# Performance work log

Measured on AMD Instinct MI355X. Metric: run time of the kernel, lower is better.

## Reference

```python
import jax, jax.numpy as jnp
import numpy as np
from jax import lax

B, S, D, H = 4, 1024, 1024, 16
DK = D // H


def setup_inputs() -> dict:
    key = jax.random.key(0)
    ks = jax.random.split(key, 8)
    s = 0.02
    return {
        "text_embeddings": jax.random.normal(ks[0], (B, S, D), jnp.float32),
        "text_mask": jnp.ones((B, S), jnp.int32),
        "W_G": jax.random.normal(ks[1], (D, D), jnp.float32) * s,
        "b_G": jnp.zeros((D,), jnp.float32),
        "Wq": jax.random.normal(ks[2], (D, D), jnp.float32) * s,
        "bq": jnp.zeros((D,), jnp.float32),
        "Wk": jax.random.normal(ks[3], (D, D), jnp.float32) * s,
        "bk": jnp.zeros((D,), jnp.float32),
        "conv_w": jax.random.normal(ks[4], (D, H, 3), jnp.float32) * s,
        "conv_b": jnp.zeros((D,), jnp.float32),
    }


def _rope_tables(seq_len, dk):
    # interleaved sinusoidal tables, each value repeated twice along feature dim
    pos = jnp.arange(seq_len, dtype=jnp.float32)[:, None]            # [S,1]
    inv = jnp.power(10000.0, -2.0 * jnp.arange(dk // 2, dtype=jnp.float32) / dk)
    ang = pos * inv                                                   # [S,DK/2]
    cos_pos = jnp.repeat(jnp.cos(ang), 2, axis=-1)[None, None]        # [1,1,S,DK]
    sin_pos = jnp.repeat(jnp.sin(ang), 2, axis=-1)[None, None]
    return cos_pos, sin_pos


def reference(text_embeddings, text_mask, W_G, b_G, Wq, bq, Wk, bk, conv_w, conv_b):
    b, s, d = text_embeddings.shape
    g = text_embeddings @ W_G + b_G                                   # [B,S,D]
    q = (g @ Wq + bq).reshape(b, s, H, DK).transpose(0, 2, 1, 3)      # [B,H,S,DK]
    k = (g @ Wk + bk).reshape(b, s, H, DK).transpose(0, 2, 1, 3)

    cos_pos, sin_pos = _rope_tables(s, DK)
    # NOTE: query rotation uses +q_odd (module does NOT negate for q), key uses -k_odd
    qw2 = jnp.stack([q[..., 1::2], q[..., ::2]], axis=-1).reshape(q.shape)
    qw = q * cos_pos + qw2 * sin_pos
    kw2 = jnp.stack([-k[..., 1::2], k[..., ::2]], axis=-1).reshape(k.shape)
    kw = k * cos_pos + kw2 * sin_pos

    scores = jnp.einsum("bhqd,bhkd->bhqk", qw, kw) / np.float32(np.sqrt(DK))
    mask = text_mask[:, None, None, :]                                # [B,1,1,S]
    scores = jnp.where(mask == 0, jnp.float32(-1e9), scores)
    p_attn = jax.nn.softmax(scores, axis=-1)                          # [B,H,S,S]

    row0 = p_attn[:, :, 0, :]                                         # [B,H,S]
    conv = lax.conv_general_dilated(
        row0, conv_w, window_strides=(1,), padding=[(1, 1)],
        dimension_numbers=("NCH", "OIH", "NCH"))                      # [B,D,S]
    return jax.nn.relu(conv + conv_b[None, :, None])
```

## Files before the change

### kernel.cpp

```cpp
#include <hip/hip_runtime.h>
#include <math.h>

#define B_  4
#define S_  1024
#define D_  1024
#define H_  16
#define DK_ 64
#define M_  (B_ * S_)

typedef __bf16 bf16x8 __attribute__((ext_vector_type(8)));
typedef float  f32x4  __attribute__((ext_vector_type(4)));

__device__ __forceinline__ unsigned short f2bf(float f) {
  unsigned u = __builtin_bit_cast(unsigned, f);
  u = (u + 0x7FFFu + ((u >> 16) & 1u)) >> 16;
  return (unsigned short)u;
}
__device__ __forceinline__ float bf2f(unsigned short h) {
  unsigned u = ((unsigned)h) << 16;
  return __builtin_bit_cast(float, u);
}

__device__ __forceinline__ void gl_lds16(const void* g, void* lds) {
  __builtin_amdgcn_global_load_lds(
      (const __attribute__((address_space(1))) unsigned int*)(unsigned long long)g,
      (__attribute__((address_space(3))) unsigned int*)(unsigned int)(unsigned long long)lds,
      16, 0, 0);
}

__global__ __launch_bounds__(256) void prep_kernel(
    const float* __restrict__ X, const float* __restrict__ W_G,
    const float* __restrict__ Wk, unsigned short* __restrict__ Xbf,
    unsigned short* __restrict__ WGT, unsigned short* __restrict__ WkT,
    float* __restrict__ tab) {
  __shared__ float tle[32][33];
  const int blk = blockIdx.x;
  const int tid = threadIdx.x;

  if (blk < 2048) {
    const int i = (blk * 256 + tid) * 2;
    const float4 v0 = ((const float4*)X)[i];
    const float4 v1 = ((const float4*)X)[i + 1];
    ushort4 h0, h1;
    h0.x = f2bf(v0.x); h0.y = f2bf(v0.y); h0.z = f2bf(v0.z); h0.w = f2bf(v0.w);
    h1.x = f2bf(v1.x); h1.y = f2bf(v1.y); h1.z = f2bf(v1.z); h1.w = f2bf(v1.w);
    ((ushort4*)Xbf)[i] = h0;
    ((ushort4*)Xbf)[i + 1] = h1;
  } else if (blk < 4096) {
    const bool isG = blk < 3072;
    const float* W = isG ? W_G : Wk;
    unsigned short* WT = isG ? WGT : WkT;
    const int t = isG ? blk - 2048 : blk - 3072;
    const int k0 = (t & 31) * 32;
    const int n0 = (t >> 5) * 32;
    const int tx = tid & 31;
    const int ty = tid >> 5;
#pragma unroll
    for (int r = 0; r < 32; r += 8)
      tle[ty + r][tx] = W[(size_t)(k0 + ty + r) * 1024 + n0 + tx];
    __syncthreads();
#pragma unroll
    for (int r = 0; r < 32; r += 8)
      WT[(size_t)(n0 + ty + r) * 1024 + k0 + tx] = f2bf(tle[tx][ty + r]);
  } else {
    const int idx = (blk - 4096) * 256 + tid;
    const int s = idx >> 5, j = idx & 31;
    const float inv = (float)exp(-(double)j * (9.210340371976182736 / 32.0));
    float sn, c;
    sincosf((float)s * inv, &sn, &c);
    tab[(size_t)s * 64 + 2 * j] = c;
    tab[(size_t)s * 64 + 2 * j + 1] = sn;
  }
}

#define GM 64
#define GN 128

__global__ __launch_bounds__(256) void gemm_bf16(
    const unsigned short* __restrict__ A, const unsigned short* __restrict__ BT,
    const float* __restrict__ bias, unsigned short* __restrict__ C,
    const float* __restrict__ Wq, float* __restrict__ part, int nGemmBlocks) {
  __shared__ __align__(16) unsigned short As[2][GM * 32];
  __shared__ __align__(16) unsigned short Bs[2][GN * 32];
  __shared__ float gs[4][32];

  const int flat = blockIdx.x;
  const int tid  = threadIdx.x;

  if (flat >= nGemmBlocks) {
    const int qb = flat - nGemmBlocks;
    const int slab = qb >> 2;
    const int n = (qb & 3) * 256 + tid;
    if (tid < 128) {
      const int b = tid >> 5, kk = tid & 31;
      gs[b][kk] = bf2f(A[(size_t)b * S_ * D_ + slab * 32 + kk]);
    }
    __syncthreads();
    float a0 = 0.f, a1 = 0.f, a2 = 0.f, a3 = 0.f;
#pragma unroll
    for (int kk = 0; kk < 32; ++kk) {
      const float w = Wq[(size_t)(slab * 32 + kk) * D_ + n];
      a0 = fmaf(gs[0][kk], w, a0);
      a1 = fmaf(gs[1][kk], w, a1);
      a2 = fmaf(gs[2][kk], w, a2);
      a3 = fmaf(gs[3][kk], w, a3);
    }
    part[(size_t)(slab * 4 + 0) * D_ + n] = a0;
    part[(size_t)(slab * 4 + 1) * D_ + n] = a1;
    part[(size_t)(slab * 4 + 2) * D_ + n] = a2;
    part[(size_t)(slab * 4 + 3) * D_ + n] = a3;
    return;
  }

  const int bx = flat & 7;
  const int by = flat >> 3;
  const int wv   = tid >> 6;
  const int lane = tid & 63;
  const int m0 = by * GM;
  const int n0 = bx * GN;

  const int colOff = (lane & 3) * 8;
  const size_t aOff  = (size_t)(m0 + 16 * wv + (lane >> 2)) * 1024 + colOff;
  const size_t bOff0 = (size_t)(n0 + 32 * wv + (lane >> 2)) * 1024 + colOff;
  const size_t bOff1 = bOff0 + (size_t)16 * 1024;

  const int l15  = lane & 15;
  const int quad = lane >> 4;

  f32x4 acc[4][2];
#pragma unroll
  for (int i = 0; i < 4; ++i)
#pragma unroll
    for (int j = 0; j < 2; ++j) acc[i][j] = (f32x4){0.f, 0.f, 0.f, 0.f};

#pragma unroll 1
  for (int k0 = 0; k0 < 1024; k0 += 64) {
    __syncthreads();
#pragma unroll
    for (int ks = 0; ks < 2; ++ks) {
      gl_lds16(A  + aOff  + k0 + ks * 32, &As[ks][wv * 512]);
      gl_lds16(BT + bOff0 + k0 + ks * 32, &Bs[ks][wv * 1024]);
      gl_lds16(BT + bOff1 + k0 + ks * 32, &Bs[ks][wv * 1024 + 512]);
    }
    __syncthreads();

#pragma unroll
    for (int ks = 0; ks < 2; ++ks) {
      bf16x8 af[4], bfr[2];
#pragma unroll
      for (int mi = 0; mi < 4; ++mi)
        af[mi] = *(const bf16x8*)(&As[ks][(mi * 16 + l15) * 32 + quad * 8]);
#pragma unroll
      for (int ni = 0; ni < 2; ++ni)
        bfr[ni] =
            *(const bf16x8*)(&Bs[ks][(wv * 32 + ni * 16 + l15) * 32 + quad * 8]);
#pragma unroll
      for (int mi = 0; mi < 4; ++mi)
#pragma unroll
        for (int ni = 0; ni < 2; ++ni)
          acc[mi][ni] = __builtin_amdgcn_mfma_f32_16x16x32_bf16(
              af[mi], bfr[ni], acc[mi][ni], 0, 0, 0);
    }
  }

#pragma unroll
  for (int ni = 0; ni < 2; ++ni) {
    const int n = n0 + wv * 32 + ni * 16 + l15;
    const float bv = bias[n];
#pragma unroll
    for (int mi = 0; mi < 4; ++mi) {
#pragma unroll
      for (int r = 0; r < 4; ++r) {
        const int m = m0 + mi * 16 + quad * 4 + r;
        C[(size_t)m * 1024 + n] = f2bf(acc[mi][ni][r] + bv);
      }
    }
  }
}

__global__ __launch_bounds__(256) void attn_scores_kernel(
    const unsigned short* __restrict__ Kbf, const float* __restrict__ part,
    const float* __restrict__ bq, const float* __restrict__ tab,
    const int* __restrict__ mask, float* __restrict__ scores,
    float* __restrict__ mS) {
  const int bi = blockIdx.x;
  const int b = bi >> 9;
  const int h = (bi >> 5) & 15;
  const int chunk = bi & 31;
  const int tid = threadIdx.x;
  const int bh = b * H_ + h;
  const int sl = tid >> 3;
  const int j  = tid & 7;
  const int s  = chunk * 32 + sl;

  __shared__ float q0s[DK_];
  __shared__ float wredm[4];
  __shared__ float wreds[4];

  if (tid < 64) {
    const int n = h * DK_ + tid;
    float v = bq[n];
#pragma unroll
    for (int sl2 = 0; sl2 < 32; ++sl2)
      v += part[(size_t)(sl2 * 4 + b) * D_ + n];
    q0s[tid] = v;
  }
  __syncthreads();

  const ushort4* kp =
      (const ushort4*)(Kbf + ((size_t)(b * S_ + s)) * D_ + h * DK_ + j * 8);
  const ushort4 k0 = kp[0], k1 = kp[1];
  const float4* tb = (const float4*)(tab + (size_t)s * 64 + j * 8);
  const float4 t0 = tb[0], t1 = tb[1];

  float dot = 0.f;
  {
    const float ka = bf2f(k0.x), kb = bf2f(k0.y);
    dot += q0s[j * 8 + 0] * (ka * t0.x - kb * t0.y) +
           q0s[j * 8 + 1] * (kb * t0.x + ka * t0.y);
  }
  {
    const float ka = bf2f(k0.z), kb = bf2f(k0.w);
    dot += q0s[j * 8 + 2] * (ka * t0.z - kb * t0.w) +
           q0s[j * 8 + 3] * (kb * t0.z + ka * t0.w);
  }
  {
    const float ka = bf2f(k1.x), kb = bf2f(k1.y);
    dot += q0s[j * 8 + 4] * (ka * t1.x - kb * t1.y) +
           q0s[j * 8 + 5] * (kb * t1.x + ka * t1.y);
  }
  {
    const float ka = bf2f(k1.z), kb = bf2f(k1.w);
    dot += q0s[j * 8 + 6] * (ka * t1.z - kb * t1.w) +
           q0s[j * 8 + 7] * (kb * t1.z + ka * t1.w);
  }
  dot += __shfl_xor(dot, 1);
  dot += __shfl_xor(dot, 2);
  dot += __shfl_xor(dot, 4);
  dot *= 0.125f;
  if (mask[b * S_ + s] == 0) dot = -1e9f;
  if (j == 0) scores[(size_t)bh * S_ + s] = dot;

  float mx = dot;
#pragma unroll
  for (int off = 8; off < 64; off <<= 1) mx = fmaxf(mx, __shfl_xor(mx, off));
  if ((tid & 63) == 0) wredm[tid >> 6] = mx;
  __syncthreads();
  mx = fmaxf(fmaxf(wredm[0], wredm[1]), fmaxf(wredm[2], wredm[3]));

  float e = (j == 0) ? expf(dot - mx) : 0.f;
#pragma unroll
  for (int off = 1; off < 64; off <<= 1) e += __shfl_xor(e, off);
  if ((tid & 63) == 0) wreds[tid >> 6] = e;
  __syncthreads();
  if (tid == 0) {
    mS[(size_t)(bh * 32 + chunk) * 2 + 0] = mx;
    mS[(size_t)(bh * 32 + chunk) * 2 + 1] =
        wreds[0] + wreds[1] + wreds[2] + wreds[3];
  }
}

__global__ __launch_bounds__(256) void conv_norm_relu_kernel(
    const float* __restrict__ scores, const float* __restrict__ mS,
    const float* __restrict__ cw, const float* __restrict__ cb,
    float* __restrict__ out) {
  const int b = blockIdx.y;
  const int s0 = blockIdx.x * 16;
  const int oz = blockIdx.z * 256;
  const int tid = threadIdx.x;

  __shared__ float msh[16], ish[16];
  __shared__ float sm[16][18];

  if (tid < 16) {
    const int bh = b * H_ + tid;
    float m = -3e38f;
#pragma unroll
    for (int c = 0; c < 32; ++c)
      m = fmaxf(m, mS[(size_t)(bh * 32 + c) * 2]);
    float S = 0.f;
#pragma unroll
    for (int c = 0; c < 32; ++c)
      S += mS[(size_t)(bh * 32 + c) * 2 + 1] *
           expf(mS[(size_t)(bh * 32 + c) * 2] - m);
    msh[tid] = m;
    ish[tid] = 1.f / S;
  }
  __syncthreads();

  for (int i = tid; i < 16 * 18; i += 256) {
    const int c = i / 18, ss = i % 18;
    const int gs = s0 - 1 + ss;
    float p = 0.f;
    if (gs >= 0 && gs < S_) {
      const int bh = b * H_ + c;
      p = expf(scores[(size_t)bh * S_ + gs] - msh[c]) * ish[c];
    }
    sm[c][ss] = p;
  }
  __syncthreads();

  const int og = tid >> 4;
  const int si = tid & 15;

  float r[16][3];
#pragma unroll
  for (int c = 0; c < 16; ++c) {
    r[c][0] = sm[c][si + 0];
    r[c][1] = sm[c][si + 1];
    r[c][2] = sm[c][si + 2];
  }

#pragma unroll 1
  for (int i = 0; i < 16; ++i) {
    const int o = oz + i * 16 + og;
    const float4* wo = (const float4*)(cw + (size_t)o * 48);
    float accv = cb[o];
#pragma unroll
    for (int q = 0; q < 12; ++q) {
      const float4 w4 = wo[q];
      const int f0 = q * 4;
      accv = fmaf(r[(f0 + 0) / 3][(f0 + 0) % 3], w4.x, accv);
      accv = fmaf(r[(f0 + 1) / 3][(f0 + 1) % 3], w4.y, accv);
      accv = fmaf(r[(f0 + 2) / 3][(f0 + 2) % 3], w4.z, accv);
      accv = fmaf(r[(f0 + 3) / 3][(f0 + 3) % 3], w4.w, accv);
    }
    out[((size_t)b * D_ + o) * S_ + s0 + si] = fmaxf(accv, 0.f);
  }
}

extern "C" void kernel_launch(void* const* d_in, const int* in_sizes, int n_in,
                              void* d_out, int out_size, void* d_ws,
                              size_t ws_size, hipStream_t stream) {
  const float* x    = (const float*)d_in[0];
  const int*   mask = (const int*)d_in[1];
  const float* W_G  = (const float*)d_in[2];
  const float* b_G  = (const float*)d_in[3];
  const float* Wq   = (const float*)d_in[4];
  const float* bq   = (const float*)d_in[5];
  const float* Wk   = (const float*)d_in[6];
  const float* bk   = (const float*)d_in[7];
  const float* cw   = (const float*)d_in[8];
  const float* cb   = (const float*)d_in[9];
  float* out = (float*)d_out;

  char* ws = (char*)d_ws;
  unsigned short* Xbf = (unsigned short*)(ws);
  unsigned short* G   = (unsigned short*)(ws + (8u << 20));
  unsigned short* Kbf = (unsigned short*)(ws + (16u << 20));
  unsigned short* WGT = (unsigned short*)(ws + (24u << 20));
  unsigned short* WkT = (unsigned short*)(ws + (26u << 20));
  float* part   = (float*)(ws + (28u << 20));
  float* ropeT  = (float*)(ws + (28u << 20) + (512u << 10));
  float* scores = (float*)(ws + (28u << 20) + (768u << 10));
  float* mS     = (float*)(ws + (28u << 20) + (1024u << 10));

  prep_kernel<<<4224, 256, 0, stream>>>(x, W_G, Wk, Xbf, WGT, WkT, ropeT);
  gemm_bf16<<<512, 256, 0, stream>>>(Xbf, WGT, b_G, G, nullptr, nullptr, 512);
  gemm_bf16<<<640, 256, 0, stream>>>(G, WkT, bk, Kbf, Wq, part, 512);
  attn_scores_kernel<<<2048, 256, 0, stream>>>(Kbf, part, bq, ropeT, mask,
                                               scores, mS);
  conv_norm_relu_kernel<<<dim3(S_ / 16, B_, 4), 256, 0, stream>>>(
      scores, mS, cw, cb, out);
}
```

Measured before the change: 163.2 us.

## Fuse all stages into one persistent kernel with grid barriers

Replaces the five separate launches (prep, two GEMMs, attention scores, conv) with a single persistent kernel of 512 blocks. Stages are separated by atomic-counter grid barriers, and each stage's work is grid-strided over the blocks. The softmax also drops its running-max subtraction and stores exp(score) and per-chunk sums directly. This removes launch gaps and the separate max reduction. The costs are barrier spin overhead, a q-projection tail that runs only on 128 blocks, and possible exp overflow for large scores.

```diff
diff --git a/kernel.cpp b/kernel.cpp
--- a/kernel.cpp
+++ b/kernel.cpp
@@ -7,6 +7,7 @@
 #define H_  16
 #define DK_ 64
 #define M_  (B_ * S_)
+#define NBLK 512
 
 typedef __bf16 bf16x8 __attribute__((ext_vector_type(8)));
 typedef float  f32x4  __attribute__((ext_vector_type(4)));
@@ -28,72 +29,167 @@
       16, 0, 0);
 }
 
-__global__ __launch_bounds__(256) void prep_kernel(
-    const float* __restrict__ X, const float* __restrict__ W_G,
-    const float* __restrict__ Wk, unsigned short* __restrict__ Xbf,
-    unsigned short* __restrict__ WGT, unsigned short* __restrict__ WkT,
-    float* __restrict__ tab) {
-  __shared__ float tle[32][33];
+__device__ __forceinline__ void grid_barrier(unsigned* ctr) {
+  __syncthreads();
+  if (threadIdx.x == 0) {
+    __threadfence();
+    atomicAdd(ctr, 1u);
+    while (__hip_atomic_load(ctr, __ATOMIC_ACQUIRE,
+                             __HIP_MEMORY_SCOPE_AGENT) < NBLK)
+      __builtin_amdgcn_s_sleep(1);
+    __threadfence();
+  }
+  __syncthreads();
+}
+
+__device__ __forceinline__ void gemm_tile(
+    const unsigned short* __restrict__ A, const unsigned short* __restrict__ BT,
+    const float* __restrict__ bias, unsigned short* __restrict__ C,
+    int flat, unsigned char* SMEM) {
+  unsigned short* As = (unsigned short*)SMEM;
+  unsigned short* Bs = (unsigned short*)(SMEM + 8192);
+
+  const int tid  = threadIdx.x;
+  const int bx = flat & 7;
+  const int by = flat >> 3;
+  const int wv   = tid >> 6;
+  const int lane = tid & 63;
+  const int m0 = by * 64;
+  const int n0 = bx * 128;
+
+  const int colOff = (lane & 3) * 8;
+  const size_t aOff  = (size_t)(m0 + 16 * wv + (lane >> 2)) * 1024 + colOff;
+  const size_t bOff0 = (size_t)(n0 + 32 * wv + (lane >> 2)) * 1024 + colOff;
+  const size_t bOff1 = bOff0 + (size_t)16 * 1024;
+
+  const int l15  = lane & 15;
+  const int quad = lane >> 4;
+
+  f32x4 acc[4][2];
+#pragma unroll
+  for (int i = 0; i < 4; ++i)
+#pragma unroll
+    for (int j = 0; j < 2; ++j) acc[i][j] = (f32x4){0.f, 0.f, 0.f, 0.f};
+
+#pragma unroll 1
+  for (int k0 = 0; k0 < 1024; k0 += 64) {
+    __syncthreads();
+#pragma unroll
+    for (int ks = 0; ks < 2; ++ks) {
+      gl_lds16(A  + aOff  + k0 + ks * 32, As + ks * 2048 + wv * 512);
+      gl_lds16(BT + bOff0 + k0 + ks * 32, Bs + ks * 4096 + wv * 1024);
+      gl_lds16(BT + bOff1 + k0 + ks * 32, Bs + ks * 4096 + wv * 1024 + 512);
+    }
+    __syncthreads();
+
+#pragma unroll
+    for (int ks = 0; ks < 2; ++ks) {
+      bf16x8 af[4], bfr[2];
+#pragma unroll
+      for (int mi = 0; mi < 4; ++mi)
+        af[mi] =
+            *(const bf16x8*)(As + ks * 2048 + (mi * 16 + l15) * 32 + quad * 8);
+#pragma unroll
+      for (int ni = 0; ni < 2; ++ni)
+        bfr[ni] = *(const bf16x8*)(Bs + ks * 4096 +
+                                   (wv * 32 + ni * 16 + l15) * 32 + quad * 8);
+#pragma unroll
+      for (int mi = 0; mi < 4; ++mi)
+#pragma unroll
+        for (int ni = 0; ni < 2; ++ni)
+          acc[mi][ni] = __builtin_amdgcn_mfma_f32_16x16x32_bf16(
+              af[mi], bfr[ni], acc[mi][ni], 0, 0, 0);
+    }
+  }
+
+#pragma unroll
+  for (int ni = 0; ni < 2; ++ni) {
+    const int n = n0 + wv * 32 + ni * 16 + l15;
+    const float bv = bias[n];
+#pragma unroll
+    for (int mi = 0; mi < 4; ++mi) {
+#pragma unroll
+      for (int r = 0; r < 4; ++r) {
+        const int m = m0 + mi * 16 + quad * 4 + r;
+        C[(size_t)m * 1024 + n] = f2bf(acc[mi][ni][r] + bv);
+      }
+    }
+  }
+}
+
+__global__ __launch_bounds__(256, 2) void mega_kernel(
+    const float* __restrict__ x, const int* __restrict__ mask,
+    const float* __restrict__ W_G, const float* __restrict__ b_G,
+    const float* __restrict__ Wq, const float* __restrict__ bq,
+    const float* __restrict__ Wk, const float* __restrict__ bk,
+    const float* __restrict__ cw, const float* __restrict__ cb,
+    unsigned short* __restrict__ Xbf, unsigned short* __restrict__ G,
+    unsigned short* __restrict__ Kbf, unsigned short* __restrict__ WGT,
+    unsigned short* __restrict__ WkT, float* __restrict__ part,
+    float* __restrict__ ropeT, float* __restrict__ scores,
+    float* __restrict__ mS, unsigned* __restrict__ bar,
+    float* __restrict__ out) {
+  __shared__ __align__(16) unsigned char SMEM[24576];
   const int blk = blockIdx.x;
   const int tid = threadIdx.x;
 
-  if (blk < 2048) {
-    const int i = (blk * 256 + tid) * 2;
-    const float4 v0 = ((const float4*)X)[i];
-    const float4 v1 = ((const float4*)X)[i + 1];
-    ushort4 h0, h1;
-    h0.x = f2bf(v0.x); h0.y = f2bf(v0.y); h0.z = f2bf(v0.z); h0.w = f2bf(v0.w);
-    h1.x = f2bf(v1.x); h1.y = f2bf(v1.y); h1.z = f2bf(v1.z); h1.w = f2bf(v1.w);
-    ((ushort4*)Xbf)[i] = h0;
-    ((ushort4*)Xbf)[i + 1] = h1;
-  } else if (blk < 4096) {
-    const bool isG = blk < 3072;
-    const float* W = isG ? W_G : Wk;
-    unsigned short* WT = isG ? WGT : WkT;
-    const int t = isG ? blk - 2048 : blk - 3072;
-    const int k0 = (t & 31) * 32;
-    const int n0 = (t >> 5) * 32;
-    const int tx = tid & 31;
-    const int ty = tid >> 5;
-#pragma unroll
-    for (int r = 0; r < 32; r += 8)
-      tle[ty + r][tx] = W[(size_t)(k0 + ty + r) * 1024 + n0 + tx];
+  {
+    float (*tle)[33] = (float(*)[33])SMEM;
+    for (int u = blk; u < 4224; u += NBLK) {
+      __syncthreads();
+      if (u < 2048) {
+        const int i = (u * 256 + tid) * 2;
+        const float4 v0 = ((const float4*)x)[i];
+        const float4 v1 = ((const float4*)x)[i + 1];
+        ushort4 h0, h1;
+        h0.x = f2bf(v0.x); h0.y = f2bf(v0.y);
+        h0.z = f2bf(v0.z); h0.w = f2bf(v0.w);
+        h1.x = f2bf(v1.x); h1.y = f2bf(v1.y);
+        h1.z = f2bf(v1.z); h1.w = f2bf(v1.w);
+        ((ushort4*)Xbf)[i] = h0;
+        ((ushort4*)Xbf)[i + 1] = h1;
+      } else if (u < 4096) {
+        const bool isG = u < 3072;
+        const float* W = isG ? W_G : Wk;
+        unsigned short* WT = isG ? WGT : WkT;
+        const int t = u - (isG ? 2048 : 3072);
+        const int k0 = (t & 31) * 32;
+        const int n0 = (t >> 5) * 32;
+        const int tx = tid & 31;
+        const int ty = tid >> 5;
+#pragma unroll
+        for (int r = 0; r < 32; r += 8)
+          tle[ty + r][tx] = W[(size_t)(k0 + ty + r) * 1024 + n0 + tx];
+        __syncthreads();
+#pragma unroll
+        for (int r = 0; r < 32; r += 8)
+          WT[(size_t)(n0 + ty + r) * 1024 + k0 + tx] = f2bf(tle[tx][ty + r]);
+      } else {
+        const int idx = (u - 4096) * 256 + tid;
+        const int s = idx >> 5, j = idx & 31;
+        const float inv =
+            (float)exp(-(double)j * (9.210340371976182736 / 32.0));
+        float sn, c;
+        sincosf((float)s * inv, &sn, &c);
+        ropeT[(size_t)s * 64 + 2 * j] = c;
+        ropeT[(size_t)s * 64 + 2 * j + 1] = sn;
+      }
+    }
+  }
+  grid_barrier(bar + 0);
+
+  gemm_tile(Xbf, WGT, b_G, G, blk, SMEM);
+  grid_barrier(bar + 1);
+
+  gemm_tile(G, WkT, bk, Kbf, blk, SMEM);
+  if (blk < 128) {
     __syncthreads();
-#pragma unroll
-    for (int r = 0; r < 32; r += 8)
-      WT[(size_t)(n0 + ty + r) * 1024 + k0 + tx] = f2bf(tle[tx][ty + r]);
-  } else {
-    const int idx = (blk - 4096) * 256 + tid;
-    const int s = idx >> 5, j = idx & 31;
-    const float inv = (float)exp(-(double)j * (9.210340371976182736 / 32.0));
-    float sn, c;
-    sincosf((float)s * inv, &sn, &c);
-    tab[(size_t)s * 64 + 2 * j] = c;
-    tab[(size_t)s * 64 + 2 * j + 1] = sn;
-  }
-}
-
-#define GM 64
-#define GN 128
-
-__global__ __launch_bounds__(256) void gemm_bf16(
-    const unsigned short* __restrict__ A, const unsigned short* __restrict__ BT,
-    const float* __restrict__ bias, unsigned short* __restrict__ C,
-    const float* __restrict__ Wq, float* __restrict__ part, int nGemmBlocks) {
-  __shared__ __align__(16) unsigned short As[2][GM * 32];
-  __shared__ __align__(16) unsigned short Bs[2][GN * 32];
-  __shared__ float gs[4][32];
-
-  const int flat = blockIdx.x;
-  const int tid  = threadIdx.x;
-
-  if (flat >= nGemmBlocks) {
-    const int qb = flat - nGemmBlocks;
-    const int slab = qb >> 2;
-    const int n = (qb & 3) * 256 + tid;
+    float (*gs)[32] = (float(*)[32])SMEM;
+    const int slab = blk >> 2;
+    const int n = (blk & 3) * 256 + tid;
     if (tid < 128) {
       const int b = tid >> 5, kk = tid & 31;
-      gs[b][kk] = bf2f(A[(size_t)b * S_ * D_ + slab * 32 + kk]);
+      gs[b][kk] = bf2f(G[(size_t)b * S_ * D_ + slab * 32 + kk]);
     }
     __syncthreads();
     float a0 = 0.f, a1 = 0.f, a2 = 0.f, a3 = 0.f;
@@ -109,223 +205,129 @@
     part[(size_t)(slab * 4 + 1) * D_ + n] = a1;
     part[(size_t)(slab * 4 + 2) * D_ + n] = a2;
     part[(size_t)(slab * 4 + 3) * D_ + n] = a3;
-    return;
-  }
-
-  const int bx = flat & 7;
-  const int by = flat >> 3;
-  const int wv   = tid >> 6;
-  const int lane = tid & 63;
-  const int m0 = by * GM;
-  const int n0 = bx * GN;
-
-  const int colOff = (lane & 3) * 8;
-  const size_t aOff  = (size_t)(m0 + 16 * wv + (lane >> 2)) * 1024 + colOff;
-  const size_t bOff0 = (size_t)(n0 + 32 * wv + (lane >> 2)) * 1024 + colOff;
-  const size_t bOff1 = bOff0 + (size_t)16 * 1024;
-
-  const int l15  = lane & 15;
-  const int quad = lane >> 4;
-
-  f32x4 acc[4][2];
-#pragma unroll
-  for (int i = 0; i < 4; ++i)
-#pragma unroll
-    for (int j = 0; j < 2; ++j) acc[i][j] = (f32x4){0.f, 0.f, 0.f, 0.f};
-
+  }
+  grid_barrier(bar + 2);
+
+  {
+    float* q0s  = (float*)SMEM;
+    float* wred = (float*)(SMEM + 256);
+    for (int u = blk; u < 2048; u += NBLK) {
+      const int b = u >> 9;
+      const int h = (u >> 5) & 15;
+      const int chunk = u & 31;
+      const int bh = b * H_ + h;
+      const int sl = tid >> 3;
+      const int j  = tid & 7;
+      const int s  = chunk * 32 + sl;
+      __syncthreads();
+      if (tid < 64) {
+        const int n = h * DK_ + tid;
+        float v = bq[n];
+#pragma unroll
+        for (int sl2 = 0; sl2 < 32; ++sl2)
+          v += part[(size_t)(sl2 * 4 + b) * D_ + n];
+        q0s[tid] = v;
+      }
+      __syncthreads();
+
+      const ushort4* kp =
+          (const ushort4*)(Kbf + ((size_t)(b * S_ + s)) * D_ + h * DK_ + j * 8);
+      const ushort4 k0v = kp[0], k1v = kp[1];
+      const float4* tb = (const float4*)(ropeT + (size_t)s * 64 + j * 8);
+      const float4 t0 = tb[0], t1 = tb[1];
+
+      float dot = 0.f;
+      {
+        const float ka = bf2f(k0v.x), kb = bf2f(k0v.y);
+        dot += q0s[j * 8 + 0] * (ka * t0.x - kb * t0.y) +
+               q0s[j * 8 + 1] * (kb * t0.x + ka * t0.y);
+      }
+      {
+        const float ka = bf2f(k0v.z), kb = bf2f(k0v.w);
+        dot += q0s[j * 8 + 2] * (ka * t0.z - kb * t0.w) +
+               q0s[j * 8 + 3] * (kb * t0.z + ka * t0.w);
+      }
+      {
+        const float ka = bf2f(k1v.x), kb = bf2f(k1v.y);
+        dot += q0s[j * 8 + 4] * (ka * t1.x - kb * t1.y) +
+               q0s[j * 8 + 5] * (kb * t1.x + ka * t1.y);
+      }
+      {
+        const float ka = bf2f(k1v.z), kb = bf2f(k1v.w);
+        dot += q0s[j * 8 + 6] * (ka * t1.z - kb * t1.w) +
+               q0s[j * 8 + 7] * (kb * t1.z + ka * t1.w);
+      }
+      dot += __shfl_xor(dot, 1);
+      dot += __shfl_xor(dot, 2);
+      dot += __shfl_xor(dot, 4);
+      dot *= 0.125f;
+      const float e = (mask[b * S_ + s] == 0) ? 0.f : expf(dot);
+      if (j == 0) scores[(size_t)bh * S_ + s] = e;
+
+      float esum = (j == 0) ? e : 0.f;
+#pragma unroll
+      for (int off = 1; off < 64; off <<= 1) esum += __shfl_xor(esum, off);
+      if ((tid & 63) == 0) wred[tid >> 6] = esum;
+      __syncthreads();
+      if (tid == 0)
+        mS[(size_t)bh * 32 + chunk] = wred[0] + wred[1] + wred[2] + wred[3];
+    }
+  }
+  grid_barrier(bar + 3);
+
+  {
+    float* ish = (float*)SMEM;
+    float (*sm)[18] = (float(*)[18])(SMEM + 64);
+    for (int u = blk; u < 1024; u += NBLK) {
+      const int xT = u & 63;
+      const int b  = (u >> 6) & 3;
+      const int oq = u >> 8;
+      const int s0 = xT * 16;
+      const int oz = oq * 256;
+      __syncthreads();
+      if (tid < 16) {
+        const int bh = b * H_ + tid;
+        float Ssum = 0.f;
+#pragma unroll
+        for (int c = 0; c < 32; ++c) Ssum += mS[(size_t)bh * 32 + c];
+        ish[tid] = 1.f / Ssum;
+      }
+      __syncthreads();
+      for (int i = tid; i < 16 * 18; i += 256) {
+        const int c = i / 18, ss = i % 18;
+        const int gs = s0 - 1 + ss;
+        sm[c][ss] = (gs >= 0 && gs < S_)
+                        ? scores[(size_t)(b * H_ + c) * S_ + gs] * ish[c]
+                        : 0.f;
+      }
+      __syncthreads();
+
+      const int og = tid >> 4;
+      const int si = tid & 15;
+      float r[16][3];
+#pragma unroll
+      for (int c = 0; c < 16; ++c) {
+        r[c][0] = sm[c][si + 0];
+        r[c][1] = sm[c][si + 1];
+        r[c][2] = sm[c][si + 2];
+      }
 #pragma unroll 1
-  for (int k0 = 0; k0 < 1024; k0 += 64) {
-    __syncthreads();
-#pragma unroll
-    for (int ks = 0; ks < 2; ++ks) {
-      gl_lds16(A  + aOff  + k0 + ks * 32, &As[ks][wv * 512]);
-      gl_lds16(BT + bOff0 + k0 + ks * 32, &Bs[ks][wv * 1024]);
-      gl_lds16(BT + bOff1 + k0 + ks * 32, &Bs[ks][wv * 1024 + 512]);
-    }
-    __syncthreads();
-
-#pragma unroll
-    for (int ks = 0; ks < 2; ++ks) {
-      bf16x8 af[4], bfr[2];
-#pragma unroll
-      for (int mi = 0; mi < 4; ++mi)
-        af[mi] = *(const bf16x8*)(&As[ks][(mi * 16 + l15) * 32 + quad * 8]);
-#pragma unroll
-      for (int ni = 0; ni < 2; ++ni)
-        bfr[ni] =
-            *(const bf16x8*)(&Bs[ks][(wv * 32 + ni * 16 + l15) * 32 + quad * 8]);
-#pragma unroll
-      for (int mi = 0; mi < 4; ++mi)
-#pragma unroll
-        for (int ni = 0; ni < 2; ++ni)
-          acc[mi][ni] = __builtin_amdgcn_mfma_f32_16x16x32_bf16(
-              af[mi], bfr[ni], acc[mi][ni], 0, 0, 0);
-    }
-  }
-
-#pragma unroll
-  for (int ni = 0; ni < 2; ++ni) {
-    const int n = n0 + wv * 32 + ni * 16 + l15;
-    const float bv = bias[n];
-#pragma unroll
-    for (int mi = 0; mi < 4; ++mi) {
-#pragma unroll
-      for (int r = 0; r < 4; ++r) {
-        const int m = m0 + mi * 16 + quad * 4 + r;
-        C[(size_t)m * 1024 + n] = f2bf(acc[mi][ni][r] + bv);
-      }
-    }
-  }
-}
-
-__global__ __launch_bounds__(256) void attn_scores_kernel(
-    const unsigned short* __restrict__ Kbf, const float* __restrict__ part,
-    const float* __restrict__ bq, const float* __restrict__ tab,
-    const int* __restrict__ mask, float* __restrict__ scores,
-    float* __restrict__ mS) {
-  const int bi = blockIdx.x;
-  const int b = bi >> 9;
-  const int h = (bi >> 5) & 15;
-  const int chunk = bi & 31;
-  const int tid = threadIdx.x;
-  const int bh = b * H_ + h;
-  const int sl = tid >> 3;
-  const int j  = tid & 7;
-  const int s  = chunk * 32 + sl;
-
-  __shared__ float q0s[DK_];
-  __shared__ float wredm[4];
-  __shared__ float wreds[4];
-
-  if (tid < 64) {
-    const int n = h * DK_ + tid;
-    float v = bq[n];
-#pragma unroll
-    for (int sl2 = 0; sl2 < 32; ++sl2)
-      v += part[(size_t)(sl2 * 4 + b) * D_ + n];
-    q0s[tid] = v;
-  }
-  __syncthreads();
-
-  const ushort4* kp =
-      (const ushort4*)(Kbf + ((size_t)(b * S_ + s)) * D_ + h * DK_ + j * 8);
-  const ushort4 k0 = kp[0], k1 = kp[1];
-  const float4* tb = (const float4*)(tab + (size_t)s * 64 + j * 8);
-  const float4 t0 = tb[0], t1 = tb[1];
-
-  float dot = 0.f;
-  {
-    const float ka = bf2f(k0.x), kb = bf2f(k0.y);
-    dot += q0s[j * 8 + 0] * (ka * t0.x - kb * t0.y) +
-           q0s[j * 8 + 1] * (kb * t0.x + ka * t0.y);
-  }
-  {
-    const float ka = bf2f(k0.z), kb = bf2f(k0.w);
-    dot += q0s[j * 8 + 2] * (ka * t0.z - kb * t0.w) +
-           q0s[j * 8 + 3] * (kb * t0.z + ka * t0.w);
-  }
-  {
-    const float ka = bf2f(k1.x), kb = bf2f(k1.y);
-    dot += q0s[j * 8 + 4] * (ka * t1.x - kb * t1.y) +
-           q0s[j * 8 + 5] * (kb * t1.x + ka * t1.y);
-  }
-  {
-    const float ka = bf2f(k1.z), kb = bf2f(k1.w);
-    dot += q0s[j * 8 + 6] * (ka * t1.z - kb * t1.w) +
-           q0s[j * 8 + 7] * (kb * t1.z + ka * t1.w);
-  }
-  dot += __shfl_xor(dot, 1);
-  dot += __shfl_xor(dot, 2);
-  dot += __shfl_xor(dot, 4);
-  dot *= 0.125f;
-  if (mask[b * S_ + s] == 0) dot = -1e9f;
-  if (j == 0) scores[(size_t)bh * S_ + s] = dot;
-
-  float mx = dot;
-#pragma unroll
-  for (int off = 8; off < 64; off <<= 1) mx = fmaxf(mx, __shfl_xor(mx, off));
-  if ((tid & 63) == 0) wredm[tid >> 6] = mx;
-  __syncthreads();
-  mx = fmaxf(fmaxf(wredm[0], wredm[1]), fmaxf(wredm[2], wredm[3]));
-
-  float e = (j == 0) ? expf(dot - mx) : 0.f;
-#pragma unroll
-  for (int off = 1; off < 64; off <<= 1) e += __shfl_xor(e, off);
-  if ((tid & 63) == 0) wreds[tid >> 6] = e;
-  __syncthreads();
-  if (tid == 0) {
-    mS[(size_t)(bh * 32 + chunk) * 2 + 0] = mx;
-    mS[(size_t)(bh * 32 + chunk) * 2 + 1] =
-        wreds[0] + wreds[1] + wreds[2] + wreds[3];
-  }
-}
-
-__global__ __launch_bounds__(256) void conv_norm_relu_kernel(
-    const float* __restrict__ scores, const float* __restrict__ mS,
-    const float* __restrict__ cw, const float* __restrict__ cb,
-    float* __restrict__ out) {
-  const int b = blockIdx.y;
-  const int s0 = blockIdx.x * 16;
-  const int oz = blockIdx.z * 256;
-  const int tid = threadIdx.x;
-
-  __shared__ float msh[16], ish[16];
-  __shared__ float sm[16][18];
-
-  if (tid < 16) {
-    const int bh = b * H_ + tid;
-    float m = -3e38f;
-#pragma unroll
-    for (int c = 0; c < 32; ++c)
-      m = fmaxf(m, mS[(size_t)(bh * 32 + c) * 2]);
-    float S = 0.f;
-#pragma unroll
-    for (int c = 0; c < 32; ++c)
-      S += mS[(size_t)(bh * 32 + c) * 2 + 1] *
-           expf(mS[(size_t)(bh * 32 + c) * 2] - m);
-    msh[tid] = m;
-    ish[tid] = 1.f / S;
-  }
-  __syncthreads();
-
-  for (int i = tid; i < 16 * 18; i += 256) {
-    const int c = i / 18, ss = i % 18;
-    const int gs = s0 - 1 + ss;
-    float p = 0.f;
-    if (gs >= 0 && gs < S_) {
-      const int bh = b * H_ + c;
-      p = expf(scores[(size_t)bh * S_ + gs] - msh[c]) * ish[c];
-    }
-    sm[c][ss] = p;
-  }
-  __syncthreads();
-
-  const int og = tid >> 4;
-  const int si = tid & 15;
-
-  float r[16][3];
-#pragma unroll
-  for (int c = 0; c < 16; ++c) {
-    r[c][0] = sm[c][si + 0];
-    r[c][1] = sm[c][si + 1];
-    r[c][2] = sm[c][si + 2];
-  }
-
-#pragma unroll 1
-  for (int i = 0; i < 16; ++i) {
-    const int o = oz + i * 16 + og;
-    const float4* wo = (const float4*)(cw + (size_t)o * 48);
-    float accv = cb[o];
-#pragma unroll
-    for (int q = 0; q < 12; ++q) {
-      const float4 w4 = wo[q];
-      const int f0 = q * 4;
-      accv = fmaf(r[(f0 + 0) / 3][(f0 + 0) % 3], w4.x, accv);
-      accv = fmaf(r[(f0 + 1) / 3][(f0 + 1) % 3], w4.y, accv);
-      accv = fmaf(r[(f0 + 2) / 3][(f0 + 2) % 3], w4.z, accv);
-      accv = fmaf(r[(f0 + 3) / 3][(f0 + 3) % 3], w4.w, accv);
-    }
-    out[((size_t)b * D_ + o) * S_ + s0 + si] = fmaxf(accv, 0.f);
+      for (int i = 0; i < 16; ++i) {
+        const int o = oz + i * 16 + og;
+        const float4* wo = (const float4*)(cw + (size_t)o * 48);
+        float accv = cb[o];
+#pragma unroll
+        for (int q = 0; q < 12; ++q) {
+          const float4 w4 = wo[q];
+          const int f0 = q * 4;
+          accv = fmaf(r[(f0 + 0) / 3][(f0 + 0) % 3], w4.x, accv);
+          accv = fmaf(r[(f0 + 1) / 3][(f0 + 1) % 3], w4.y, accv);
+          accv = fmaf(r[(f0 + 2) / 3][(f0 + 2) % 3], w4.z, accv);
+          accv = fmaf(r[(f0 + 3) / 3][(f0 + 3) % 3], w4.w, accv);
+        }
+        out[((size_t)b * D_ + o) * S_ + s0 + si] = fmaxf(accv, 0.f);
+      }
+    }
   }
 }
 
@@ -354,12 +356,10 @@
   float* ropeT  = (float*)(ws + (28u << 20) + (512u << 10));
   float* scores = (float*)(ws + (28u << 20) + (768u << 10));
   float* mS     = (float*)(ws + (28u << 20) + (1024u << 10));
-
-  prep_kernel<<<4224, 256, 0, stream>>>(x, W_G, Wk, Xbf, WGT, WkT, ropeT);
-  gemm_bf16<<<512, 256, 0, stream>>>(Xbf, WGT, b_G, G, nullptr, nullptr, 512);
-  gemm_bf16<<<640, 256, 0, stream>>>(G, WkT, bk, Kbf, Wq, part, 512);
-  attn_scores_kernel<<<2048, 256, 0, stream>>>(Kbf, part, bq, ropeT, mask,
-                                               scores, mS);
-  conv_norm_relu_kernel<<<dim3(S_ / 16, B_, 4), 256, 0, stream>>>(
-      scores, mS, cw, cb, out);
-}
+  unsigned* bar = (unsigned*)(ws + (30u << 20));
+
+  hipMemsetAsync(bar, 0, 64, stream);
+  mega_kernel<<<NBLK, 256, 0, stream>>>(x, mask, W_G, b_G, Wq, bq, Wk, bk, cw,
+                                        cb, Xbf, G, Kbf, WGT, WkT, part, ropeT,
+                                        scores, mS, bar, out);
+}
```

After: 425.7 us. +160.8%, slower.

## Fuse RoPE scores and softmax sums into the K GEMM epilogue

Applied to the files above, without the earlier changes.

Row 0 of G is now computed in fp32 by extra prep blocks. The query row is then built by extra blocks in the first GEMM launch instead of in slab partials. The K projection GEMM no longer writes K to memory: its epilogue applies RoPE, takes the dot product with the query row, exponentiates, and adds the softmax denominators into a per-(batch, head) buffer with atomics. This removes the separate attention-scores kernel, the large K write and read-back, and the partial-sum reduction, at the cost of skipping max subtraction in the softmax, which relies on the scores staying small.

```diff
diff --git a/kernel.cpp b/kernel.cpp
--- a/kernel.cpp
+++ b/kernel.cpp
@@ -30,10 +30,13 @@
 
 __global__ __launch_bounds__(256) void prep_kernel(
     const float* __restrict__ X, const float* __restrict__ W_G,
-    const float* __restrict__ Wk, unsigned short* __restrict__ Xbf,
-    unsigned short* __restrict__ WGT, unsigned short* __restrict__ WkT,
-    float* __restrict__ tab) {
+    const float* __restrict__ Wk, const float* __restrict__ b_G,
+    unsigned short* __restrict__ Xbf, unsigned short* __restrict__ WGT,
+    unsigned short* __restrict__ WkT, float* __restrict__ tab,
+    float* __restrict__ gr0) {
   __shared__ float tle[32][33];
+  __shared__ float xs[1024];
+  __shared__ float pall[256];
   const int blk = blockIdx.x;
   const int tid = threadIdx.x;
 
@@ -62,7 +65,7 @@
 #pragma unroll
     for (int r = 0; r < 32; r += 8)
       WT[(size_t)(n0 + ty + r) * 1024 + k0 + tx] = f2bf(tle[tx][ty + r]);
-  } else {
+  } else if (blk < 4224) {
     const int idx = (blk - 4096) * 256 + tid;
     const int s = idx >> 5, j = idx & 31;
     const float inv = (float)exp(-(double)j * (9.210340371976182736 / 32.0));
@@ -70,6 +73,24 @@
     sincosf((float)s * inv, &sn, &c);
     tab[(size_t)s * 64 + 2 * j] = c;
     tab[(size_t)s * 64 + 2 * j + 1] = sn;
+  } else {
+    const int u = blk - 4224;
+    const int b = u >> 4;
+    const int n0g = (u & 15) * 64;
+    const int nl = tid & 63;
+    const int kq = tid >> 6;
+    for (int i = tid; i < 1024; i += 256) xs[i] = X[(size_t)b * S_ * D_ + i];
+    __syncthreads();
+    float acc = 0.f;
+    const int ks = kq * 256;
+    for (int k = ks; k < ks + 256; ++k)
+      acc = fmaf(xs[k], W_G[(size_t)k * 1024 + n0g + nl], acc);
+    pall[tid] = acc;
+    __syncthreads();
+    if (tid < 64)
+      gr0[(size_t)b * 1024 + n0g + tid] = pall[tid] + pall[64 + tid] +
+                                          pall[128 + tid] + pall[192 + tid] +
+                                          b_G[n0g + tid];
   }
 }
 
@@ -79,36 +100,59 @@
 __global__ __launch_bounds__(256) void gemm_bf16(
     const unsigned short* __restrict__ A, const unsigned short* __restrict__ BT,
     const float* __restrict__ bias, unsigned short* __restrict__ C,
-    const float* __restrict__ Wq, float* __restrict__ part, int nGemmBlocks) {
+    const float* __restrict__ gr0, const float* __restrict__ Wq,
+    const float* __restrict__ bq, float* __restrict__ q0,
+    const float* __restrict__ tab, const int* __restrict__ mask,
+    float* __restrict__ scores, float* __restrict__ mS, int mode) {
   __shared__ __align__(16) unsigned short As[2][GM * 32];
   __shared__ __align__(16) unsigned short Bs[2][GN * 32];
-  __shared__ float gs[4][32];
+  __shared__ float schalf[4 * GM];
 
   const int flat = blockIdx.x;
   const int tid  = threadIdx.x;
 
-  if (flat >= nGemmBlocks) {
-    const int qb = flat - nGemmBlocks;
-    const int slab = qb >> 2;
-    const int n = (qb & 3) * 256 + tid;
-    if (tid < 128) {
-      const int b = tid >> 5, kk = tid & 31;
-      gs[b][kk] = bf2f(A[(size_t)b * S_ * D_ + slab * 32 + kk]);
-    }
-    __syncthreads();
+  if (flat >= 512) {
+    float* gs   = (float*)As;
+    float* pall = (float*)Bs;
+    float* gs2   = (float*)Bs;
+    float* pall2 = ((float*)Bs) + 2048;
+    const int u = flat - 512;
+    const int n0q = u * 64;
+    const int nl = tid & 63;
+    const int kq = tid >> 6;
+    if (u == 0 && tid < 64) mS[tid] = 0.f;
+    for (int i = tid; i < 2048; i += 256) gs[i] = gr0[i];
+    for (int i = tid; i < 2048; i += 256) gs2[i] = gr0[2048 + i];
+    __syncthreads();
+    const int ks = kq * 256;
     float a0 = 0.f, a1 = 0.f, a2 = 0.f, a3 = 0.f;
-#pragma unroll
-    for (int kk = 0; kk < 32; ++kk) {
-      const float w = Wq[(size_t)(slab * 32 + kk) * D_ + n];
-      a0 = fmaf(gs[0][kk], w, a0);
-      a1 = fmaf(gs[1][kk], w, a1);
-      a2 = fmaf(gs[2][kk], w, a2);
-      a3 = fmaf(gs[3][kk], w, a3);
-    }
-    part[(size_t)(slab * 4 + 0) * D_ + n] = a0;
-    part[(size_t)(slab * 4 + 1) * D_ + n] = a1;
-    part[(size_t)(slab * 4 + 2) * D_ + n] = a2;
-    part[(size_t)(slab * 4 + 3) * D_ + n] = a3;
+    for (int k = ks; k < ks + 256; ++k) {
+      const float w = Wq[(size_t)k * 1024 + n0q + nl];
+      a0 = fmaf(gs[k], w, a0);
+      a1 = fmaf(gs[1024 + k], w, a1);
+      a2 = fmaf(gs2[k], w, a2);
+      a3 = fmaf(gs2[1024 + k], w, a3);
+    }
+    __syncthreads();
+    pall2[tid] = a0;
+    pall2[256 + tid] = a1;
+    schalf[tid % 256 < 256 ? 0 : 0] = schalf[0];
+    float* pallA = pall2;
+    float* pallB = ((float*)As);
+    pallB[tid] = a2;
+    pallB[256 + tid] = a3;
+    __syncthreads();
+    if (tid < 64) {
+      const float bqv = bq[n0q + tid];
+      q0[(size_t)0 * 1024 + n0q + tid] = pallA[tid] + pallA[64 + tid] +
+                                         pallA[128 + tid] + pallA[192 + tid] + bqv;
+      q0[(size_t)1 * 1024 + n0q + tid] = pallA[256 + tid] + pallA[320 + tid] +
+                                         pallA[384 + tid] + pallA[448 + tid] + bqv;
+      q0[(size_t)2 * 1024 + n0q + tid] = pallB[tid] + pallB[64 + tid] +
+                                         pallB[128 + tid] + pallB[192 + tid] + bqv;
+      q0[(size_t)3 * 1024 + n0q + tid] = pallB[256 + tid] + pallB[320 + tid] +
+                                         pallB[384 + tid] + pallB[448 + tid] + bqv;
+    }
     return;
   }
 
@@ -163,100 +207,82 @@
     }
   }
 
-#pragma unroll
-  for (int ni = 0; ni < 2; ++ni) {
-    const int n = n0 + wv * 32 + ni * 16 + l15;
-    const float bv = bias[n];
-#pragma unroll
-    for (int mi = 0; mi < 4; ++mi) {
-#pragma unroll
-      for (int r = 0; r < 4; ++r) {
-        const int m = m0 + mi * 16 + quad * 4 + r;
-        C[(size_t)m * 1024 + n] = f2bf(acc[mi][ni][r] + bv);
+  if (mode == 1) {
+#pragma unroll
+    for (int ni = 0; ni < 2; ++ni) {
+      const int n = n0 + wv * 32 + ni * 16 + l15;
+      const float bv = bias[n];
+#pragma unroll
+      for (int mi = 0; mi < 4; ++mi) {
+#pragma unroll
+        for (int r = 0; r < 4; ++r) {
+          const int m = m0 + mi * 16 + quad * 4 + r;
+          C[(size_t)m * 1024 + n] = f2bf(acc[mi][ni][r] + bv);
+        }
       }
     }
-  }
-}
-
-__global__ __launch_bounds__(256) void attn_scores_kernel(
-    const unsigned short* __restrict__ Kbf, const float* __restrict__ part,
-    const float* __restrict__ bq, const float* __restrict__ tab,
-    const int* __restrict__ mask, float* __restrict__ scores,
-    float* __restrict__ mS) {
-  const int bi = blockIdx.x;
-  const int b = bi >> 9;
-  const int h = (bi >> 5) & 15;
-  const int chunk = bi & 31;
-  const int tid = threadIdx.x;
-  const int bh = b * H_ + h;
-  const int sl = tid >> 3;
-  const int j  = tid & 7;
-  const int s  = chunk * 32 + sl;
-
-  __shared__ float q0s[DK_];
-  __shared__ float wredm[4];
-  __shared__ float wreds[4];
-
-  if (tid < 64) {
-    const int n = h * DK_ + tid;
-    float v = bq[n];
-#pragma unroll
-    for (int sl2 = 0; sl2 < 32; ++sl2)
-      v += part[(size_t)(sl2 * 4 + b) * D_ + n];
-    q0s[tid] = v;
+    return;
+  }
+
+  const int b = m0 >> 10;
+  const int s0 = m0 & 1023;
+  const int nA = n0 + wv * 32 + l15;
+  const int nB = nA + 16;
+  const float bkA = bias[nA], bkB = bias[nB];
+  const float qA = q0[(size_t)b * 1024 + nA];
+  const float qB = q0[(size_t)b * 1024 + nB];
+  const int dkA = nA & 63, dkB = nB & 63;
+  const int odd = dkA & 1;
+  const int baseA = dkA & ~1, baseB = dkB & ~1;
+
+  float pm[16];
+#pragma unroll
+  for (int mi = 0; mi < 4; ++mi) {
+#pragma unroll
+    for (int r = 0; r < 4; ++r) {
+      const int s = s0 + mi * 16 + quad * 4 + r;
+      const float vA = acc[mi][0][r] + bkA;
+      const float vB = acc[mi][1][r] + bkB;
+      const float pA = __shfl_xor(vA, 1);
+      const float pB = __shfl_xor(vB, 1);
+      const float2 tA = *(const float2*)&tab[(size_t)s * 64 + baseA];
+      const float2 tB = *(const float2*)&tab[(size_t)s * 64 + baseB];
+      const float kwA = odd ? (vA * tA.x + pA * tA.y) : (vA * tA.x - pA * tA.y);
+      const float kwB = odd ? (vB * tB.x + pB * tB.y) : (vB * tB.x - pB * tB.y);
+      pm[mi * 4 + r] = kwA * qA + kwB * qB;
+    }
+  }
+#pragma unroll
+  for (int i = 0; i < 16; ++i) {
+    pm[i] += __shfl_xor(pm[i], 1);
+    pm[i] += __shfl_xor(pm[i], 2);
+    pm[i] += __shfl_xor(pm[i], 4);
+    pm[i] += __shfl_xor(pm[i], 8);
   }
   __syncthreads();
-
-  const ushort4* kp =
-      (const ushort4*)(Kbf + ((size_t)(b * S_ + s)) * D_ + h * DK_ + j * 8);
-  const ushort4 k0 = kp[0], k1 = kp[1];
-  const float4* tb = (const float4*)(tab + (size_t)s * 64 + j * 8);
-  const float4 t0 = tb[0], t1 = tb[1];
-
-  float dot = 0.f;
-  {
-    const float ka = bf2f(k0.x), kb = bf2f(k0.y);
-    dot += q0s[j * 8 + 0] * (ka * t0.x - kb * t0.y) +
-           q0s[j * 8 + 1] * (kb * t0.x + ka * t0.y);
-  }
-  {
-    const float ka = bf2f(k0.z), kb = bf2f(k0.w);
-    dot += q0s[j * 8 + 2] * (ka * t0.z - kb * t0.w) +
-           q0s[j * 8 + 3] * (kb * t0.z + ka * t0.w);
-  }
-  {
-    const float ka = bf2f(k1.x), kb = bf2f(k1.y);
-    dot += q0s[j * 8 + 4] * (ka * t1.x - kb * t1.y) +
-           q0s[j * 8 + 5] * (kb * t1.x + ka * t1.y);
-  }
-  {
-    const float ka = bf2f(k1.z), kb = bf2f(k1.w);
-    dot += q0s[j * 8 + 6] * (ka * t1.z - kb * t1.w) +
-           q0s[j * 8 + 7] * (kb * t1.z + ka * t1.w);
-  }
-  dot += __shfl_xor(dot, 1);
-  dot += __shfl_xor(dot, 2);
-  dot += __shfl_xor(dot, 4);
-  dot *= 0.125f;
-  if (mask[b * S_ + s] == 0) dot = -1e9f;
-  if (j == 0) scores[(size_t)bh * S_ + s] = dot;
-
-  float mx = dot;
-#pragma unroll
-  for (int off = 8; off < 64; off <<= 1) mx = fmaxf(mx, __shfl_xor(mx, off));
-  if ((tid & 63) == 0) wredm[tid >> 6] = mx;
+  if (l15 == 0) {
+#pragma unroll
+    for (int mi = 0; mi < 4; ++mi)
+#pragma unroll
+      for (int r = 0; r < 4; ++r)
+        schalf[wv * GM + mi * 16 + quad * 4 + r] = pm[mi * 4 + r];
+  }
   __syncthreads();
-  mx = fmaxf(fmaxf(wredm[0], wredm[1]), fmaxf(wredm[2], wredm[3]));
-
-  float e = (j == 0) ? expf(dot - mx) : 0.f;
-#pragma unroll
-  for (int off = 1; off < 64; off <<= 1) e += __shfl_xor(e, off);
-  if ((tid & 63) == 0) wreds[tid >> 6] = e;
-  __syncthreads();
-  if (tid == 0) {
-    mS[(size_t)(bh * 32 + chunk) * 2 + 0] = mx;
-    mS[(size_t)(bh * 32 + chunk) * 2 + 1] =
-        wreds[0] + wreds[1] + wreds[2] + wreds[3];
+  if (tid < 128) {
+    const int ml = tid & 63;
+    const int hsel = tid >> 6;
+    const int head = 2 * bx + hsel;
+    const int bh = b * H_ + head;
+    const int s = s0 + ml;
+    const float dot =
+        (schalf[(hsel * 2) * GM + ml] + schalf[(hsel * 2 + 1) * GM + ml]) *
+        0.125f;
+    const float e = (mask[b * S_ + s] == 0) ? 0.f : expf(dot);
+    scores[(size_t)bh * S_ + s] = e;
+    float esum = e;
+#pragma unroll
+    for (int off = 1; off < 64; off <<= 1) esum += __shfl_xor(esum, off);
+    if (ml == 0) atomicAdd(&mS[bh], esum);
   }
 }
 
@@ -269,34 +295,18 @@
   const int oz = blockIdx.z * 256;
   const int tid = threadIdx.x;
 
-  __shared__ float msh[16], ish[16];
+  __shared__ float ish[16];
   __shared__ float sm[16][18];
 
-  if (tid < 16) {
-    const int bh = b * H_ + tid;
-    float m = -3e38f;
-#pragma unroll
-    for (int c = 0; c < 32; ++c)
-      m = fmaxf(m, mS[(size_t)(bh * 32 + c) * 2]);
-    float S = 0.f;
-#pragma unroll
-    for (int c = 0; c < 32; ++c)
-      S += mS[(size_t)(bh * 32 + c) * 2 + 1] *
-           expf(mS[(size_t)(bh * 32 + c) * 2] - m);
-    msh[tid] = m;
-    ish[tid] = 1.f / S;
-  }
+  if (tid < 16) ish[tid] = 1.f / mS[b * H_ + tid];
   __syncthreads();
 
   for (int i = tid; i < 16 * 18; i += 256) {
     const int c = i / 18, ss = i % 18;
     const int gs = s0 - 1 + ss;
-    float p = 0.f;
-    if (gs >= 0 && gs < S_) {
-      const int bh = b * H_ + c;
-      p = expf(scores[(size_t)bh * S_ + gs] - msh[c]) * ish[c];
-    }
-    sm[c][ss] = p;
+    sm[c][ss] = (gs >= 0 && gs < S_)
+                    ? scores[(size_t)(b * H_ + c) * S_ + gs] * ish[c]
+                    : 0.f;
   }
   __syncthreads();
 
@@ -347,19 +357,20 @@
   char* ws = (char*)d_ws;
   unsigned short* Xbf = (unsigned short*)(ws);
   unsigned short* G   = (unsigned short*)(ws + (8u << 20));
-  unsigned short* Kbf = (unsigned short*)(ws + (16u << 20));
-  unsigned short* WGT = (unsigned short*)(ws + (24u << 20));
-  unsigned short* WkT = (unsigned short*)(ws + (26u << 20));
-  float* part   = (float*)(ws + (28u << 20));
-  float* ropeT  = (float*)(ws + (28u << 20) + (512u << 10));
-  float* scores = (float*)(ws + (28u << 20) + (768u << 10));
-  float* mS     = (float*)(ws + (28u << 20) + (1024u << 10));
-
-  prep_kernel<<<4224, 256, 0, stream>>>(x, W_G, Wk, Xbf, WGT, WkT, ropeT);
-  gemm_bf16<<<512, 256, 0, stream>>>(Xbf, WGT, b_G, G, nullptr, nullptr, 512);
-  gemm_bf16<<<640, 256, 0, stream>>>(G, WkT, bk, Kbf, Wq, part, 512);
-  attn_scores_kernel<<<2048, 256, 0, stream>>>(Kbf, part, bq, ropeT, mask,
-                                               scores, mS);
+  unsigned short* WGT = (unsigned short*)(ws + (16u << 20));
+  unsigned short* WkT = (unsigned short*)(ws + (18u << 20));
+  float* gr0    = (float*)(ws + (20u << 20));
+  float* q0     = (float*)(ws + (20u << 20) + (16u << 10));
+  float* ropeT  = (float*)(ws + (20u << 20) + (32u << 10));
+  float* scores = (float*)(ws + (20u << 20) + (288u << 10));
+  float* mS     = (float*)(ws + (20u << 20) + (544u << 10));
+
+  prep_kernel<<<4288, 256, 0, stream>>>(x, W_G, Wk, b_G, Xbf, WGT, WkT, ropeT,
+                                        gr0);
+  gemm_bf16<<<528, 256, 0, stream>>>(Xbf, WGT, b_G, G, gr0, Wq, bq, q0, ropeT,
+                                     mask, scores, mS, 1);
+  gemm_bf16<<<512, 256, 0, stream>>>(G, WkT, bk, nullptr, gr0, Wq, bq, q0,
+                                     ropeT, mask, scores, mS, 0);
   conv_norm_relu_kernel<<<dim3(S_ / 16, B_, 4), 256, 0, stream>>>(
       scores, mS, cw, cb, out);
 }
```

Result: slower. 274.7 us (+68.3%).
